# Performance work log

Hardware: AMD Instinct MI355X
Metric: run time of the kernel (lower is better)

## Reference

```python
import jax, jax.numpy as jnp
import numpy as np

B, L, C, S, W, R = 2, 16, 64, 64, 128, 32
MOD_HIDDEN = 32


def _conv3d(x, k, b, pad_hw):
    # x: (B,C,L,S,W), k: (O,I,1,kh,kw)
    y = jax.lax.conv_general_dilated(
        x, k, window_strides=(1, 1, 1),
        padding=((0, 0), (pad_hw, pad_hw), (pad_hw, pad_hw)),
        dimension_numbers=('NCDHW', 'OIDHW', 'NCDHW'))
    return y + b[None, :, None, None, None]


def setup_inputs() -> dict:
    key = jax.random.key(0)
    ks = jax.random.split(key, 16)
    d = {}
    d['x'] = jax.random.normal(ks[0], (B, L, C, S, W), jnp.float32)
    u1 = jax.random.uniform(ks[1], (C, R), jnp.float32)
    u2 = jax.random.uniform(ks[2], (C, R), jnp.float32)
    r_min, r_max = 0.8, 0.99
    d['nu_log'] = jnp.log(-0.5 * jnp.log(u1 * (r_max ** 2 - r_min ** 2) + r_min ** 2))
    d['theta_log'] = jnp.log(u2 * jnp.float32(2 * np.pi))
    d['disp_nu'] = jnp.zeros((C, R), jnp.float32)
    d['disp_theta'] = jnp.zeros((C, R), jnp.float32)
    d['mlp_w1'] = jax.random.normal(ks[3], (C, MOD_HIDDEN), jnp.float32) / np.sqrt(C).astype(np.float32)
    d['mlp_b1'] = jnp.zeros((MOD_HIDDEN,), jnp.float32)
    d['mlp_w2'] = jax.random.normal(ks[4], (MOD_HIDDEN, C * R * 2), jnp.float32) / np.sqrt(MOD_HIDDEN).astype(np.float32)
    d['mlp_b2'] = jnp.zeros((C * R * 2,), jnp.float32)
    d['forcing_scale'] = jnp.float32(0.1)
    d['U_row_r'] = jax.random.normal(ks[5], (C, S, R), jnp.float32) / np.sqrt(S).astype(np.float32)
    d['U_row_i'] = jax.random.normal(ks[6], (C, S, R), jnp.float32) / np.sqrt(S).astype(np.float32)
    d['V_col_r'] = jax.random.normal(ks[7], (C, W, R), jnp.float32) / np.sqrt(W).astype(np.float32)
    d['V_col_i'] = jax.random.normal(ks[8], (C, W, R), jnp.float32) / np.sqrt(W).astype(np.float32)
    d['proj_W_r'] = jax.random.normal(ks[9], (C, C), jnp.float32) / np.sqrt(C).astype(np.float32)
    d['proj_W_i'] = jax.random.normal(ks[10], (C, C), jnp.float32) / np.sqrt(C).astype(np.float32)
    d['proj_b_r'] = jnp.zeros((C,), jnp.float32)
    d['proj_b_i'] = jnp.zeros((C,), jnp.float32)
    fan = np.sqrt(C * 9).astype(np.float32)
    d['convr_k'] = jax.random.normal(ks[11], (C, C, 1, 3, 3), jnp.float32) / fan
    d['convr_b'] = jnp.zeros((C,), jnp.float32)
    d['convi_k'] = jax.random.normal(ks[12], (C, C, 1, 3, 3), jnp.float32) / fan
    d['convi_b'] = jnp.zeros((C,), jnp.float32)
    d['fuse_k'] = jax.random.normal(ks[13], (C, 2 * C, 1, 1, 1), jnp.float32) / np.sqrt(2 * C).astype(np.float32)
    d['fuse_b'] = jnp.zeros((C,), jnp.float32)
    d['ln_g'] = jnp.ones((S, W), jnp.float32)
    d['ln_b'] = jnp.zeros((S, W), jnp.float32)
    return d


def reference(x, nu_log, theta_log, disp_nu, disp_theta, mlp_w1, mlp_b1,
              mlp_w2, mlp_b2, forcing_scale, U_row_r, U_row_i, V_col_r,
              V_col_i, proj_W_r, proj_W_i, proj_b_r, proj_b_i, convr_k,
              convr_b, convi_k, convi_b, fuse_k, fuse_b, ln_g, ln_b):
    # Diagonal LRU poles lam = exp(-exp(nu) + i*exp(theta)), per (C,R)
    nu = jnp.exp(nu_log + disp_nu)
    theta = jnp.exp(theta_log + disp_theta)
    lam = jnp.exp(jax.lax.complex(-nu, theta))
    gamma = jnp.sqrt(jnp.clip(1.0 - jnp.abs(lam) ** 2, 1e-6, None))

    # Selective input-dependent forcing from spatially-pooled context
    ctx = x.mean(axis=(-2, -1))  # (B,L,C)
    f = jnp.tanh(ctx @ mlp_w1 + mlp_b1) @ mlp_w2 + mlp_b2
    f = f.reshape(ctx.shape[0], ctx.shape[1], C, R, 2)
    forcing = forcing_scale * jax.lax.complex(f[..., 0], f[..., 1])  # (B,L,C,R)

    # Low-rank complex spatial projection to rank-R state per channel
    U = jax.lax.complex(U_row_r, U_row_i)  # (C,S,R)
    V = jax.lax.complex(V_col_r, V_col_i)  # (C,W,R)
    xc = x.astype(jnp.complex64)
    u = jnp.einsum('blcsw,csr->blcwr', xc, jnp.conj(U))
    u = jnp.einsum('blcwr,cwr->blcr', u, jnp.conj(V))  # (B,L,C,R)
    u = gamma * u * (1.0 + forcing)

    # Diagonal linear recurrence h_t = lam*h_{t-1} + u_t via associative scan over L
    A = jnp.broadcast_to(lam[None, None], u.shape)

    def comb(e1, e2):
        a1, b1 = e1
        a2, b2 = e2
        return a1 * a2, a2 * b1 + b2

    _, h = jax.lax.associative_scan(comb, (A, u), axis=1)

    # Reconstruct spatial field from low-rank states
    t = jnp.einsum('blcr,csr->blcsr', h, U)
    y = jnp.einsum('blcsr,cwr->blcsw', t, V)  # (B,L,C,S,W) complex

    projW = jax.lax.complex(proj_W_r, proj_W_i)
    projb = jax.lax.complex(proj_b_r, proj_b_i)
    y = jnp.einsum('blcsw,oc->blosw', y, projW) + projb[None, None, :, None, None]

    # Post-recurrence spatial convs on real/imag parts, fuse, layernorm, residual
    yr = jnp.transpose(jnp.real(y), (0, 2, 1, 3, 4))  # (B,C,L,S,W)
    yi = jnp.transpose(jnp.imag(y), (0, 2, 1, 3, 4))
    yr = _conv3d(yr, convr_k, convr_b, 1)
    yi = _conv3d(yi, convi_k, convi_b, 1)
    fused = _conv3d(jnp.concatenate([yr, yi], axis=1), fuse_k, fuse_b, 0)
    fused = jnp.transpose(fused, (0, 2, 1, 3, 4))  # (B,L,C,S,W)

    mu = fused.mean(axis=(-2, -1), keepdims=True)
    var = fused.var(axis=(-2, -1), keepdims=True)
    normed = (fused - mu) / jnp.sqrt(var + 1e-5) * ln_g + ln_b
    return normed + x
```

## Files before the change

kernel.cpp:

```cpp
#include <hip/hip_runtime.h>

typedef unsigned short u16;
typedef unsigned int u32;
typedef __attribute__((ext_vector_type(8))) short short8;
typedef __attribute__((ext_vector_type(4))) float f32x4;
typedef __attribute__((ext_vector_type(16))) float f32x16;

constexpr int B = 2, L = 16, C = 64, S = 64, W = 128, R = 32, MH = 32;
constexpr int BL = B * L;
constexpr int SW = S * W;
constexpr int CR = C * R;
constexpr int F2 = C * R * 2;

__device__ __forceinline__ float us2f(u16 h) { return __uint_as_float(((u32)h) << 16); }
__device__ __forceinline__ float bf_lo(u32 u) { return __uint_as_float(u << 16); }
__device__ __forceinline__ float bf_hi(u32 u) { return __uint_as_float(u & 0xffff0000u); }
__device__ __forceinline__ u16 f2bu(float f) {
  u32 u = __float_as_uint(f);
  u32 r = (u + 0x7fffu + ((u >> 16) & 1u)) >> 16;
  return (u16)r;
}
__device__ __forceinline__ u32 pack2(float lo, float hi) {
  return (u32)f2bu(lo) | ((u32)f2bu(hi) << 16);
}

__global__ void k_prep(const float* __restrict__ nu_log, const float* __restrict__ th_log,
                       const float* __restrict__ dnu, const float* __restrict__ dth,
                       float* __restrict__ lamr, float* __restrict__ lami,
                       float* __restrict__ gam) {
  int i = blockIdx.x * 256 + threadIdx.x;
  if (i >= CR) return;
  float nu = expf(nu_log[i] + dnu[i]);
  float th = expf(th_log[i] + dth[i]);
  float mag = expf(-nu);
  lamr[i] = mag * cosf(th);
  lami[i] = mag * sinf(th);
  gam[i] = sqrtf(fmaxf(1.0f - mag * mag, 1e-6f));
}

__global__ void k_keff(const float* __restrict__ fuse_k, const float* __restrict__ fuse_b,
                       const float* __restrict__ convr_k, const float* __restrict__ convr_b,
                       const float* __restrict__ convi_k, const float* __restrict__ convi_b,
                       u16* __restrict__ keff_bf, float* __restrict__ biaseff) {
  int i = blockIdx.x * 256 + threadIdx.x;
  if (i < C * 2 * C * 9) {
    int o = i / (2 * C * 9);
    int rem = i - o * (2 * C * 9);
    int cin2 = rem / 9;
    int seg = rem - cin2 * 9;
    const float* ck = (cin2 < C) ? convr_k : convi_k;
    int cin = cin2 & (C - 1);
    int fbase = o * 2 * C + ((cin2 < C) ? 0 : C);
    float acc = 0.f;
    for (int m = 0; m < C; ++m)
      acc += fuse_k[fbase + m] * ck[(m * C + cin) * 9 + seg];
    int kslice = cin2 >> 4;
    int kk = cin2 & 15;
    int lane = (o & 31) | ((kk >> 3) << 5);
    int j = kk & 7;
    int m_tile = o >> 5;
    keff_bf[((((seg * 8 + kslice) * 2 + m_tile) * 64 + lane) << 3) + j] = f2bu(acc);
  } else if (i < C * 2 * C * 9 + C) {
    int o = i - C * 2 * C * 9;
    float acc = fuse_b[o];
    for (int m = 0; m < C; ++m) {
      acc += fuse_k[o * 2 * C + m] * convr_b[m];
      acc += fuse_k[o * 2 * C + C + m] * convi_b[m];
    }
    biaseff[o] = acc;
  }
}

__global__ void k_apack(const float* __restrict__ pWr, const float* __restrict__ pWi,
                        u16* __restrict__ aproj) {
  int i = blockIdx.x * 256 + threadIdx.x;
  if (i >= 128 * 128) return;
  int m = i >> 7, k = i & 127;
  int c = k >> 1, im = k & 1;
  int o = m & 63;
  float v;
  if (m < 64) v = im ? -pWi[o * 64 + c] : pWr[o * 64 + c];
  else        v = im ?  pWr[o * 64 + c] : pWi[o * 64 + c];
  aproj[i] = f2bu(v);
}

__global__ __launch_bounds__(256) void k_mlp(
    const float* __restrict__ ctx, const float* __restrict__ w1, const float* __restrict__ b1,
    const float* __restrict__ w2, const float* __restrict__ b2, const float* __restrict__ fscale,
    float* __restrict__ forcing) {
  int bl = blockIdx.x >> 4;
  int kt = blockIdx.x & 15;
  int k0 = kt * 256;
  __shared__ float cv[C];
  __shared__ float hid[MH];
  __shared__ float lw2[MH * 256];
  int t = threadIdx.x;
  if (t < C) cv[t] = ctx[bl * C + t];
  for (int i = t; i < MH * 64; i += 256) {
    int j = i >> 6, q = i & 63;
    ((float4*)lw2)[i] = ((const float4*)(w2 + (size_t)j * F2 + k0))[q];
  }
  __syncthreads();
  if (t < MH) {
    float a = b1[t];
    for (int c2 = 0; c2 < C; ++c2) a += cv[c2] * w1[c2 * MH + t];
    hid[t] = tanhf(a);
  }
  __syncthreads();
  float scale = fscale[0];
  float a = b2[k0 + t];
#pragma unroll
  for (int j = 0; j < MH; ++j) a += hid[j] * lw2[j * 256 + t];
  forcing[(size_t)bl * F2 + k0 + t] = scale * a;
}

__global__ __launch_bounds__(256) void k_enc(
    const float* __restrict__ x,
    const float* __restrict__ Vr, const float* __restrict__ Vi,
    const float* __restrict__ Ur, const float* __restrict__ Ui,
    float* __restrict__ ctx, float* __restrict__ u) {
  int blc = blockIdx.x;
  int c = blc & (C - 1);
  __shared__ __align__(16) char smem[17408 * 2 + 16384 + 64];
  u16* xt = (u16*)smem;
  u16* bt = (u16*)(smem + 17408);
  float* uldr = (float*)(smem + 34816);
  float* uldi = uldr + 2048;
  float* y1  = (float*)smem;
  float* part = (float*)(smem + 17408);
  float* red = (float*)(smem + 17408 * 2 + 16384);
  int t = threadIdx.x;
  int lane = t & 63, wv = t >> 6;
  float sm = 0.f;
  {
    const float4* xp = (const float4*)(x + (size_t)blc * SW);
    for (int i = t; i < SW / 4; i += 256) {
      float4 v = xp[i];
      sm += v.x + v.y + v.z + v.w;
      int idx = i * 4, s = idx >> 7, w = idx & 127;
      u32* d = (u32*)&xt[s * 136 + w];
      d[0] = pack2(v.x, v.y);
      d[1] = pack2(v.z, v.w);
    }
  }
#pragma unroll
  for (int o = 32; o > 0; o >>= 1) sm += __shfl_down(sm, o, 64);
  if (lane == 0) red[wv] = sm;
  {
    const float* vrp = Vr + (size_t)c * 4096;
    const float* vip = Vi + (size_t)c * 4096;
    for (int i = t; i < 4096; i += 256) {
      int w = i >> 5, r = i & 31;
      bt[r * 136 + w]        = f2bu(vrp[i]);
      bt[(32 + r) * 136 + w] = f2bu(-vip[i]);
    }
  }
  {
    const float* urp = Ur + (size_t)c * 2048;
    const float* uip = Ui + (size_t)c * 2048;
    for (int i = t; i < 2048; i += 256) { uldr[i] = urp[i]; uldi[i] = uip[i]; }
  }
  __syncthreads();
  if (t == 0) ctx[blc] = (red[0] + red[1] + red[2] + red[3]) * (1.f / SW);
  int quad = lane >> 4, l15 = lane & 15;
  f32x4 zf = {0.f, 0.f, 0.f, 0.f};
  f32x4 acc[4] = {zf, zf, zf, zf};
#pragma unroll
  for (int ks = 0; ks < 4; ++ks) {
    int kofs = ks * 32 + quad * 8;
    short8 bf = *(const short8*)&bt[(wv * 16 + l15) * 136 + kofs];
#pragma unroll
    for (int mt = 0; mt < 4; ++mt) {
      short8 af = *(const short8*)&xt[(mt * 16 + l15) * 136 + kofs];
      acc[mt] = __builtin_amdgcn_mfma_f32_16x16x32_bf16(af, bf, acc[mt], 0, 0, 0);
    }
  }
  __syncthreads();
#pragma unroll
  for (int mt = 0; mt < 4; ++mt)
#pragma unroll
    for (int reg = 0; reg < 4; ++reg)
      y1[(mt * 16 + quad * 4 + reg) * 65 + wv * 16 + l15] = acc[mt][reg];
  __syncthreads();
  {
    int r = t & 31, sg = t >> 5;
    float pr = 0.f, pi = 0.f;
#pragma unroll
    for (int k = 0; k < 8; ++k) {
      int s = sg * 8 + k;
      float yr = y1[s * 65 + r], yi = y1[s * 65 + 32 + r];
      float ur = uldr[s * 32 + r], ui = uldi[s * 32 + r];
      pr += ur * yr + ui * yi;
      pi += ur * yi - ui * yr;
    }
    part[sg * 64 + r * 2]     = pr;
    part[sg * 64 + r * 2 + 1] = pi;
  }
  __syncthreads();
  if (t < 32) {
    float pr = 0.f, pi = 0.f;
#pragma unroll
    for (int sg = 0; sg < 8; ++sg) {
      pr += part[sg * 64 + t * 2];
      pi += part[sg * 64 + t * 2 + 1];
    }
    u[((size_t)blc * R + t) * 2]     = pr;
    u[((size_t)blc * R + t) * 2 + 1] = pi;
  }
}

__global__ void k_scan(const float* __restrict__ lamr, const float* __restrict__ lami,
                       const float* __restrict__ gam, const float* __restrict__ forcing,
                       const float* __restrict__ u, float* __restrict__ h) {
  int i = blockIdx.x * 256 + threadIdx.x;
  if (i >= B * CR) return;
  int b = i / CR;
  int cr = i - b * CR;
  float lr = lamr[cr], li = lami[cr], g = gam[cr];
  float hr = 0.f, hi = 0.f;
  for (int l = 0; l < L; ++l) {
    size_t off = ((size_t)(b * L + l) * CR + cr) * 2;
    float ur0 = u[off], ui0 = u[off + 1];
    float fr = forcing[off], fi = forcing[off + 1];
    float ofr = 1.f + fr;
    float ur = g * (ur0 * ofr - ui0 * fi);
    float ui = g * (ur0 * fi + ui0 * ofr);
    float nr = lr * hr - li * hi + ur;
    float ni = lr * hi + li * hr + ui;
    hr = nr; hi = ni;
    h[off] = hr; h[off + 1] = hi;
  }
}

__global__ __launch_bounds__(256) void k_decode(
    const float* __restrict__ h,
    const float* __restrict__ Ur, const float* __restrict__ Ui,
    const float* __restrict__ Vr, const float* __restrict__ Vi,
    u32* __restrict__ y_cm32, int bl_base) {
  int bid = blockIdx.x;
  int c = bid & 63;
  int blh = bid >> 6;
  int bl = bl_base + blh;
  __shared__ __align__(16) u16 ldA[64 * 72];
  __shared__ __align__(16) u16 ldBr[128 * 72];
  __shared__ __align__(16) u16 ldBi[128 * 72];
  int t = threadIdx.x;
  {
    const float* hp = h + ((size_t)(bl * C + c) * R) * 2;
    const float* urp = Ur + (size_t)c * (S * R);
    const float* uip = Ui + (size_t)c * (S * R);
    for (int p = t; p < S * R; p += 256) {
      int s = p >> 5, r = p & 31;
      float hr = hp[r * 2], hi = hp[r * 2 + 1];
      float ur = urp[p], ui = uip[p];
      ldA[s * 72 + r]      = f2bu(hr * ur - hi * ui);
      ldA[s * 72 + 32 + r] = f2bu(hr * ui + hi * ur);
    }
  }
  {
    const float* vrp = Vr + (size_t)c * (W * R);
    const float* vip = Vi + (size_t)c * (W * R);
    for (int p = t; p < W * R; p += 256) {
      int w = p >> 5, r = p & 31;
      float vr = vrp[p], vi = vip[p];
      ldBr[w * 72 + r]      = f2bu(vr);
      ldBr[w * 72 + 32 + r] = f2bu(-vi);
      ldBi[w * 72 + r]      = f2bu(vi);
      ldBi[w * 72 + 32 + r] = f2bu(vr);
    }
  }
  __syncthreads();
  int lane = t & 63, q = t >> 6;
  int quad = lane >> 4, l15 = lane & 15;
  f32x4 zf = {0.f, 0.f, 0.f, 0.f};
  f32x4 accr[4][2], acci[4][2];
#pragma unroll
  for (int mt = 0; mt < 4; ++mt)
#pragma unroll
    for (int nt = 0; nt < 2; ++nt) { accr[mt][nt] = zf; acci[mt][nt] = zf; }
#pragma unroll
  for (int ks = 0; ks < 2; ++ks) {
    int kofs = ks * 32 + quad * 8;
    short8 af[4];
#pragma unroll
    for (int mt = 0; mt < 4; ++mt)
      af[mt] = *(const short8*)&ldA[(mt * 16 + l15) * 72 + kofs];
#pragma unroll
    for (int nt = 0; nt < 2; ++nt) {
      int wrow = q * 32 + nt * 16 + l15;
      short8 br = *(const short8*)&ldBr[wrow * 72 + kofs];
      short8 bi = *(const short8*)&ldBi[wrow * 72 + kofs];
#pragma unroll
      for (int mt = 0; mt < 4; ++mt) {
        accr[mt][nt] = __builtin_amdgcn_mfma_f32_16x16x32_bf16(af[mt], br, accr[mt][nt], 0, 0, 0);
        acci[mt][nt] = __builtin_amdgcn_mfma_f32_16x16x32_bf16(af[mt], bi, acci[mt][nt], 0, 0, 0);
      }
    }
  }
  u32* dst = y_cm32 + ((size_t)(blh * 64 + c) << 13);
#pragma unroll
  for (int mt = 0; mt < 4; ++mt) {
#pragma unroll
    for (int nt = 0; nt < 2; ++nt) {
      int w = q * 32 + nt * 16 + l15;
#pragma unroll
      for (int reg = 0; reg < 4; ++reg) {
        int s = mt * 16 + quad * 4 + reg;
        dst[s * 128 + w] = pack2(accr[mt][nt][reg], acci[mt][nt][reg]);
      }
    }
  }
}

__global__ __launch_bounds__(256) void k_proj(
    const u32* __restrict__ y_cm32, const u16* __restrict__ aproj,
    const float* __restrict__ pbr, const float* __restrict__ pbi,
    u16* __restrict__ ynhwc, int bl_base) {
  int bid = blockIdx.x;
  int ntile = bid & 15;
  int blh = bid >> 4;
  int bl = bl_base + blh;
  __shared__ __align__(16) u16 lda[128 * 136];
  __shared__ __align__(16) u32 ldb[128 * 68];
  __shared__ float ldbias[128];
  int t = threadIdx.x;
  for (int i = t; i < 128 * 16; i += 256) {
    int m = i >> 4, qq = i & 15;
    ((uint4*)&lda[m * 136])[qq] = ((const uint4*)&aproj[m * 128])[qq];
  }
  if (t < 128) ldbias[t] = t < 64 ? pbr[t] : pbi[t - 64];

  int lane = t & 63, wv = t >> 6;
  int quad = lane >> 4, l15 = lane & 15;
  int cidx = t & 63, seg = t >> 6;
  f32x4 zf = {0.f, 0.f, 0.f, 0.f};

  for (int chunk = 0; chunk < 4; ++chunk) {
    int n0 = ntile * 512 + chunk * 128;
    __syncthreads();
    {
      const uint4* src = (const uint4*)(y_cm32 + (((size_t)(blh * 64 + cidx)) << 13) + n0 + seg * 32);
      u32 tmp[32];
#pragma unroll
      for (int qq = 0; qq < 8; ++qq) {
        uint4 v = src[qq];
        tmp[qq * 4] = v.x; tmp[qq * 4 + 1] = v.y; tmp[qq * 4 + 2] = v.z; tmp[qq * 4 + 3] = v.w;
      }
#pragma unroll
      for (int j = 0; j < 32; ++j)
        ldb[(seg * 32 + j) * 68 + cidx] = tmp[j];
    }
    __syncthreads();
    f32x4 acc[8][2];
#pragma unroll
    for (int mt = 0; mt < 8; ++mt) { acc[mt][0] = zf; acc[mt][1] = zf; }
    const u16* ldb16 = (const u16*)ldb;
#pragma unroll
    for (int ks = 0; ks < 4; ++ks) {
      int kofs = ks * 32 + quad * 8;
      short8 af[8];
#pragma unroll
      for (int mt = 0; mt < 8; ++mt)
        af[mt] = *(const short8*)&lda[(mt * 16 + l15) * 136 + kofs];
#pragma unroll
      for (int nt = 0; nt < 2; ++nt) {
        int nrow = wv * 32 + nt * 16 + l15;
        short8 bf = *(const short8*)&ldb16[nrow * 136 + kofs];
#pragma unroll
        for (int mt = 0; mt < 8; ++mt)
          acc[mt][nt] = __builtin_amdgcn_mfma_f32_16x16x32_bf16(af[mt], bf, acc[mt][nt], 0, 0, 0);
      }
    }
#pragma unroll
    for (int nt = 0; nt < 2; ++nt) {
      int n = n0 + wv * 32 + nt * 16 + l15;
      u16* drow = ynhwc + (((size_t)bl * SW + n) << 7);
#pragma unroll
      for (int mt = 0; mt < 8; ++mt) {
        int ch = mt * 16 + quad * 4;
        u32 lo = pack2(acc[mt][nt][0] + ldbias[ch],     acc[mt][nt][1] + ldbias[ch + 1]);
        u32 hi = pack2(acc[mt][nt][2] + ldbias[ch + 2], acc[mt][nt][3] + ldbias[ch + 3]);
        u32* dp = (u32*)(drow + ch);
        dp[0] = lo; dp[1] = hi;
      }
    }
  }
}

__global__ __launch_bounds__(256, 4) void k_conv(
    const u16* __restrict__ ynhwc, const u16* __restrict__ keff_bf,
    const float* __restrict__ biaseff, u16* __restrict__ fused) {
  int bid = blockIdx.x;
  int wt = bid & 1;
  int st = (bid >> 1) & 31;
  int bl = bid >> 6;
  int s0 = st * 2;
  int w0 = wt * 64;
  __shared__ __align__(16) u16 win[4][66][72];
  int t = threadIdx.x;
  int c_lo = (wt == 0) ? 1 : 0;
  int c_hi = (wt == 0) ? 66 : 65;
  uint4 z4 = make_uint4(0u, 0u, 0u, 0u);

  int lane = t & 63;
  int wv = t >> 6;
  int sr = wv & 1;
  int mt = wv >> 1;
  int l31 = lane & 31, khalf = lane >> 5;

  f32x16 acc0, acc1;
#pragma unroll
  for (int i = 0; i < 16; ++i) { acc0[i] = 0.f; acc1[i] = 0.f; }
  const short8* ap = (const short8*)keff_bf;
  short8 abuf[2];

#pragma unroll
  for (int p = 0; p < 2; ++p) {
    if (p) __syncthreads();
    for (int rr = 0; rr < 4; ++rr) {
      int rs = s0 - 1 + rr;
      if (rs < 0 || rs >= S) {
        for (int i = t; i < 66 * 8; i += 256) {
          int col = i >> 3, q = i & 7;
          ((uint4*)&win[rr][col][0])[q] = z4;
        }
      } else {
        if (wt == 0 && t < 8) ((uint4*)&win[rr][0][0])[t] = z4;
        if (wt == 1 && t < 8) ((uint4*)&win[rr][65][0])[t] = z4;
        const uint4* src = (const uint4*)(ynhwc +
            (((size_t)bl * S + rs) * W + (w0 - 1 + c_lo)) * 128 + p * 64);
        int n4 = (c_hi - c_lo) * 8;
        for (int i = t; i < n4; i += 256) {
          int col = i >> 3, q = i & 7;
          ((uint4*)&win[rr][c_lo + col][0])[q] = src[col * 16 + q];
        }
      }
    }
    __syncthreads();

    abuf[0] = ap[((p * 4) * 2 + mt) * 64 + lane];

#pragma unroll
    for (int m = 0; m < 36; ++m) {
      const int cur = m & 1;
      const int nxt = cur ^ 1;
      if (m < 35) {
        const int m1 = m + 1;
        abuf[nxt] = ap[((((m1 >> 2) * 8 + p * 4 + (m1 & 3)) * 2 + mt)) * 64 + lane];
      }
      const int seg = m >> 2;
      const int k4 = m & 3;
      const int dr = seg / 3;
      const int dc = seg - dr * 3;
      const u16* bb = &win[sr + dr][l31 + dc][k4 * 16 + khalf * 8];
      short8 b0 = *(const short8*)bb;
      short8 b1 = *(const short8*)(bb + 32 * 72);
      acc0 = __builtin_amdgcn_mfma_f32_32x32x16_bf16(abuf[cur], b0, acc0, 0, 0, 0);
      acc1 = __builtin_amdgcn_mfma_f32_32x32x16_bf16(abuf[cur], b1, acc1, 0, 0, 0);
    }
  }

  int s_out = s0 + sr;
#pragma unroll
  for (int reg = 0; reg < 16; ++reg) {
    int o = mt * 32 + (reg & 3) + 8 * (reg >> 2) + 4 * khalf;
    float bias = biaseff[o];
    size_t rowoff = ((size_t)(bl * C + o) * S + s_out) * W;
    fused[rowoff + w0 + l31]      = f2bu(acc0[reg] + bias);
    fused[rowoff + w0 + 32 + l31] = f2bu(acc1[reg] + bias);
  }
}

__global__ __launch_bounds__(256) void k_ln(
    const u16* __restrict__ fused,
    const float* __restrict__ ln_g, const float* __restrict__ ln_b,
    const float* __restrict__ x, float* __restrict__ out) {
  int blc = blockIdx.x;
  __shared__ u16 fs[SW];
  __shared__ float red[12];
  int t = threadIdx.x;
  const uint4* fp = (const uint4*)(fused + (size_t)blc * SW);
  float sm = 0.f, sq = 0.f;
  for (int i = t; i < SW / 8; i += 256) {
    uint4 v = fp[i];
    ((uint4*)fs)[i] = v;
    float f0 = bf_lo(v.x), f1 = bf_hi(v.x), f2 = bf_lo(v.y), f3 = bf_hi(v.y);
    float f4 = bf_lo(v.z), f5 = bf_hi(v.z), f6 = bf_lo(v.w), f7 = bf_hi(v.w);
    sm += f0 + f1 + f2 + f3 + f4 + f5 + f6 + f7;
    sq += f0 * f0 + f1 * f1 + f2 * f2 + f3 * f3 + f4 * f4 + f5 * f5 + f6 * f6 + f7 * f7;
  }
#pragma unroll
  for (int off = 32; off > 0; off >>= 1) {
    sm += __shfl_down(sm, off, 64);
    sq += __shfl_down(sq, off, 64);
  }
  int lane = t & 63, wid = t >> 6;
  if (lane == 0) { red[wid * 2] = sm; red[wid * 2 + 1] = sq; }
  __syncthreads();
  if (t == 0) {
    float S1 = red[0] + red[2] + red[4] + red[6];
    float S2 = red[1] + red[3] + red[5] + red[7];
    float mu = S1 * (1.f / SW);
    float var = S2 * (1.f / SW) - mu * mu;
    red[8] = mu;
    red[9] = rsqrtf(var + 1e-5f);
  }
  __syncthreads();
  float mu = red[8], rstd = red[9];
  const float4* xp4 = (const float4*)(x + (size_t)blc * SW);
  float4* op4 = (float4*)(out + (size_t)blc * SW);
  const float4* g4 = (const float4*)ln_g;
  const float4* b4 = (const float4*)ln_b;
  const uint2* fs2 = (const uint2*)fs;
  for (int i = t; i < SW / 4; i += 256) {
    uint2 fv = fs2[i];
    float4 xv = xp4[i];
    float4 gv = g4[i];
    float4 bv = b4[i];
    float4 o;
    o.x = (bf_lo(fv.x) - mu) * rstd * gv.x + bv.x + xv.x;
    o.y = (bf_hi(fv.x) - mu) * rstd * gv.y + bv.y + xv.y;
    o.z = (bf_lo(fv.y) - mu) * rstd * gv.z + bv.z + xv.z;
    o.w = (bf_hi(fv.y) - mu) * rstd * gv.w + bv.w + xv.w;
    op4[i] = o;
  }
}

extern "C" void kernel_launch(void* const* d_in, const int* in_sizes, int n_in,
                              void* d_out, int out_size, void* d_ws, size_t ws_size,
                              hipStream_t stream) {
  (void)in_sizes; (void)n_in; (void)out_size; (void)ws_size;
  const float* x       = (const float*)d_in[0];
  const float* nu_log  = (const float*)d_in[1];
  const float* th_log  = (const float*)d_in[2];
  const float* dnu     = (const float*)d_in[3];
  const float* dth     = (const float*)d_in[4];
  const float* w1      = (const float*)d_in[5];
  const float* b1      = (const float*)d_in[6];
  const float* w2      = (const float*)d_in[7];
  const float* b2      = (const float*)d_in[8];
  const float* fscale  = (const float*)d_in[9];
  const float* Ur      = (const float*)d_in[10];
  const float* Ui      = (const float*)d_in[11];
  const float* Vr      = (const float*)d_in[12];
  const float* Vi      = (const float*)d_in[13];
  const float* pWr     = (const float*)d_in[14];
  const float* pWi     = (const float*)d_in[15];
  const float* pbr     = (const float*)d_in[16];
  const float* pbi     = (const float*)d_in[17];
  const float* convr_k = (const float*)d_in[18];
  const float* convr_b = (const float*)d_in[19];
  const float* convi_k = (const float*)d_in[20];
  const float* convi_b = (const float*)d_in[21];
  const float* fuse_k  = (const float*)d_in[22];
  const float* fuse_b  = (const float*)d_in[23];
  const float* ln_g    = (const float*)d_in[24];
  const float* ln_b    = (const float*)d_in[25];
  float* out = (float*)d_out;

  char* ws = (char*)d_ws;
  float* lamr    = (float*)ws;
  float* lami    = lamr + 2048;
  float* gam     = lami + 2048;
  float* biaseff = gam + 2048;
  float* ctx     = biaseff + 64;
  float* forcing = ctx + 2048;
  float* ubuf    = forcing + 131072;
  float* hbuf    = ubuf + 131072;
  u16* keff_bf   = (u16*)(hbuf + 131072);
  u16* aproj     = keff_bf + 73728;
  size_t off = ((size_t)((char*)(aproj + 16384) - ws) + 255) & ~(size_t)255;
  u32* y_cm32    = (u32*)(ws + off);
  u16* fused     = (u16*)y_cm32;
  u16* ynhwc     = (u16*)(ws + off + (size_t)32 * 1024 * 1024);

  k_prep<<<8, 256, 0, stream>>>(nu_log, th_log, dnu, dth, lamr, lami, gam);
  k_keff<<<289, 256, 0, stream>>>(fuse_k, fuse_b, convr_k, convr_b, convi_k, convi_b,
                                  keff_bf, biaseff);
  k_apack<<<64, 256, 0, stream>>>(pWr, pWi, aproj);
  k_enc<<<BL * C, 256, 0, stream>>>(x, Vr, Vi, Ur, Ui, ctx, ubuf);
  k_mlp<<<BL * 16, 256, 0, stream>>>(ctx, w1, b1, w2, b2, fscale, forcing);
  k_scan<<<16, 256, 0, stream>>>(lamr, lami, gam, forcing, ubuf, hbuf);
  k_decode<<<1024, 256, 0, stream>>>(hbuf, Ur, Ui, Vr, Vi, y_cm32, 0);
  k_proj<<<256, 256, 0, stream>>>(y_cm32, aproj, pbr, pbi, ynhwc, 0);
  k_decode<<<1024, 256, 0, stream>>>(hbuf, Ur, Ui, Vr, Vi, y_cm32, 16);
  k_proj<<<256, 256, 0, stream>>>(y_cm32, aproj, pbr, pbi, ynhwc, 16);
  k_conv<<<2048, 256, 0, stream>>>(ynhwc, keff_bf, biaseff, fused);
  k_ln<<<BL * C, 256, 0, stream>>>(fused, ln_g, ln_b, x, out);
}
```

Baseline: 344.0 us.

## Prepack V weights into MFMA fragment layout once, load directly in enc/decode

Adds a k_vpack kernel that converts Vr/Vi to bf16 and arranges them in the exact per-lane MFMA B-fragment order for both the encoder and the decoder. k_enc and k_decode now load those fragments straight from global memory into registers. This removes the per-block fp32 load, convert and LDS transpose of V that was repeated across 2048 blocks each, and it shrinks LDS use. The cost is one extra launch of 6144 blocks and some extra workspace.

```diff
diff --git a/kernel.cpp b/kernel.cpp
--- a/kernel.cpp
+++ b/kernel.cpp
@@ -11,6 +11,8 @@
 constexpr int SW = S * W;
 constexpr int CR = C * R;
 constexpr int F2 = C * R * 2;
+constexpr int NVE = 64 * 4 * 4 * 64 * 8;
+constexpr int NVD = 64 * 8 * 2 * 64 * 8;
 
 __device__ __forceinline__ float us2f(u16 h) { return __uint_as_float(((u32)h) << 16); }
 __device__ __forceinline__ float bf_lo(u32 u) { return __uint_as_float(u << 16); }
@@ -71,6 +73,35 @@
   }
 }
 
+__global__ void k_vpack(const float* __restrict__ Vr, const float* __restrict__ Vi,
+                        u16* __restrict__ venc, u16* __restrict__ vdecr,
+                        u16* __restrict__ vdeci) {
+  int i = blockIdx.x * 256 + threadIdx.x;
+  if (i < NVE) {
+    int j = i & 7, lane = (i >> 3) & 63, ks = (i >> 9) & 3;
+    int wv = (i >> 11) & 3, c = i >> 13;
+    int n = wv * 16 + (lane & 15);
+    int w = ks * 32 + ((lane >> 4) & 3) * 8 + j;
+    float v = (n < 32) ? Vr[(size_t)c * 4096 + w * 32 + n]
+                       : -Vi[(size_t)c * 4096 + w * 32 + (n - 32)];
+    venc[i] = f2bu(v);
+  } else if (i < NVE + 2 * NVD) {
+    int ii = i - NVE;
+    int isI = 0;
+    if (ii >= NVD) { ii -= NVD; isI = 1; }
+    int j = ii & 7, lane = (ii >> 3) & 63, ks = (ii >> 9) & 1;
+    int g = (ii >> 10) & 7, c = ii >> 13;
+    int w = g * 16 + (lane & 15);
+    int k = ks * 32 + ((lane >> 4) & 3) * 8 + j;
+    float v;
+    if (!isI) v = (k < 32) ? Vr[(size_t)c * 4096 + w * 32 + k]
+                           : -Vi[(size_t)c * 4096 + w * 32 + (k - 32)];
+    else      v = (k < 32) ? Vi[(size_t)c * 4096 + w * 32 + k]
+                           :  Vr[(size_t)c * 4096 + w * 32 + (k - 32)];
+    (isI ? vdeci : vdecr)[ii] = f2bu(v);
+  }
+}
+
 __global__ void k_apack(const float* __restrict__ pWr, const float* __restrict__ pWi,
                         u16* __restrict__ aproj) {
   int i = blockIdx.x * 256 + threadIdx.x;
@@ -115,22 +146,26 @@
 }
 
 __global__ __launch_bounds__(256) void k_enc(
-    const float* __restrict__ x,
-    const float* __restrict__ Vr, const float* __restrict__ Vi,
+    const float* __restrict__ x, const u16* __restrict__ venc,
     const float* __restrict__ Ur, const float* __restrict__ Ui,
     float* __restrict__ ctx, float* __restrict__ u) {
   int blc = blockIdx.x;
   int c = blc & (C - 1);
-  __shared__ __align__(16) char smem[17408 * 2 + 16384 + 64];
+  __shared__ __align__(16) char smem[35968];
   u16* xt = (u16*)smem;
-  u16* bt = (u16*)(smem + 17408);
-  float* uldr = (float*)(smem + 34816);
+  float* uldr = (float*)(smem + 17408);
   float* uldi = uldr + 2048;
   float* y1  = (float*)smem;
-  float* part = (float*)(smem + 17408);
-  float* red = (float*)(smem + 17408 * 2 + 16384);
+  float* part = (float*)(smem + 33792);
+  float* red = (float*)(smem + 35840);
   int t = threadIdx.x;
   int lane = t & 63, wv = t >> 6;
+  short8 bf[4];
+  {
+    const short8* vep = (const short8*)venc + ((size_t)(c * 4 + wv) * 4) * 64 + lane;
+#pragma unroll
+    for (int ks = 0; ks < 4; ++ks) bf[ks] = vep[ks * 64];
+  }
   float sm = 0.f;
   {
     const float4* xp = (const float4*)(x + (size_t)blc * SW);
@@ -147,15 +182,6 @@
   for (int o = 32; o > 0; o >>= 1) sm += __shfl_down(sm, o, 64);
   if (lane == 0) red[wv] = sm;
   {
-    const float* vrp = Vr + (size_t)c * 4096;
-    const float* vip = Vi + (size_t)c * 4096;
-    for (int i = t; i < 4096; i += 256) {
-      int w = i >> 5, r = i & 31;
-      bt[r * 136 + w]        = f2bu(vrp[i]);
-      bt[(32 + r) * 136 + w] = f2bu(-vip[i]);
-    }
-  }
-  {
     const float* urp = Ur + (size_t)c * 2048;
     const float* uip = Ui + (size_t)c * 2048;
     for (int i = t; i < 2048; i += 256) { uldr[i] = urp[i]; uldi[i] = uip[i]; }
@@ -168,11 +194,10 @@
 #pragma unroll
   for (int ks = 0; ks < 4; ++ks) {
     int kofs = ks * 32 + quad * 8;
-    short8 bf = *(const short8*)&bt[(wv * 16 + l15) * 136 + kofs];
 #pragma unroll
     for (int mt = 0; mt < 4; ++mt) {
       short8 af = *(const short8*)&xt[(mt * 16 + l15) * 136 + kofs];
-      acc[mt] = __builtin_amdgcn_mfma_f32_16x16x32_bf16(af, bf, acc[mt], 0, 0, 0);
+      acc[mt] = __builtin_amdgcn_mfma_f32_16x16x32_bf16(af, bf[ks], acc[mt], 0, 0, 0);
     }
   }
   __syncthreads();
@@ -235,15 +260,13 @@
 __global__ __launch_bounds__(256) void k_decode(
     const float* __restrict__ h,
     const float* __restrict__ Ur, const float* __restrict__ Ui,
-    const float* __restrict__ Vr, const float* __restrict__ Vi,
+    const u16* __restrict__ vdecr, const u16* __restrict__ vdeci,
     u32* __restrict__ y_cm32, int bl_base) {
   int bid = blockIdx.x;
   int c = bid & 63;
   int blh = bid >> 6;
   int bl = bl_base + blh;
   __shared__ __align__(16) u16 ldA[64 * 72];
-  __shared__ __align__(16) u16 ldBr[128 * 72];
-  __shared__ __align__(16) u16 ldBi[128 * 72];
   int t = threadIdx.x;
   {
     const float* hp = h + ((size_t)(bl * C + c) * R) * 2;
@@ -257,21 +280,11 @@
       ldA[s * 72 + 32 + r] = f2bu(hr * ui + hi * ur);
     }
   }
-  {
-    const float* vrp = Vr + (size_t)c * (W * R);
-    const float* vip = Vi + (size_t)c * (W * R);
-    for (int p = t; p < W * R; p += 256) {
-      int w = p >> 5, r = p & 31;
-      float vr = vrp[p], vi = vip[p];
-      ldBr[w * 72 + r]      = f2bu(vr);
-      ldBr[w * 72 + 32 + r] = f2bu(-vi);
-      ldBi[w * 72 + r]      = f2bu(vi);
-      ldBi[w * 72 + 32 + r] = f2bu(vr);
-    }
-  }
   __syncthreads();
   int lane = t & 63, q = t >> 6;
   int quad = lane >> 4, l15 = lane & 15;
+  const short8* vdr = (const short8*)vdecr + (size_t)c * 16 * 64;
+  const short8* vdi = (const short8*)vdeci + (size_t)c * 16 * 64;
   f32x4 zf = {0.f, 0.f, 0.f, 0.f};
   f32x4 accr[4][2], acci[4][2];
 #pragma unroll
@@ -287,9 +300,9 @@
       af[mt] = *(const short8*)&ldA[(mt * 16 + l15) * 72 + kofs];
 #pragma unroll
     for (int nt = 0; nt < 2; ++nt) {
-      int wrow = q * 32 + nt * 16 + l15;
-      short8 br = *(const short8*)&ldBr[wrow * 72 + kofs];
-      short8 bi = *(const short8*)&ldBi[wrow * 72 + kofs];
+      int g = q * 2 + nt;
+      short8 br = vdr[(g * 2 + ks) * 64 + lane];
+      short8 bi = vdi[(g * 2 + ks) * 64 + lane];
 #pragma unroll
       for (int mt = 0; mt < 4; ++mt) {
         accr[mt][nt] = __builtin_amdgcn_mfma_f32_16x16x32_bf16(af[mt], br, accr[mt][nt], 0, 0, 0);
@@ -569,7 +582,10 @@
   float* hbuf    = ubuf + 131072;
   u16* keff_bf   = (u16*)(hbuf + 131072);
   u16* aproj     = keff_bf + 73728;
-  size_t off = ((size_t)((char*)(aproj + 16384) - ws) + 255) & ~(size_t)255;
+  u16* venc      = aproj + 16384;
+  u16* vdecr     = venc + NVE;
+  u16* vdeci     = vdecr + NVD;
+  size_t off = ((size_t)((char*)(vdeci + NVD) - ws) + 255) & ~(size_t)255;
   u32* y_cm32    = (u32*)(ws + off);
   u16* fused     = (u16*)y_cm32;
   u16* ynhwc     = (u16*)(ws + off + (size_t)32 * 1024 * 1024);
@@ -577,13 +593,14 @@
   k_prep<<<8, 256, 0, stream>>>(nu_log, th_log, dnu, dth, lamr, lami, gam);
   k_keff<<<289, 256, 0, stream>>>(fuse_k, fuse_b, convr_k, convr_b, convi_k, convi_b,
                                   keff_bf, biaseff);
+  k_vpack<<<6144, 256, 0, stream>>>(Vr, Vi, venc, vdecr, vdeci);
   k_apack<<<64, 256, 0, stream>>>(pWr, pWi, aproj);
-  k_enc<<<BL * C, 256, 0, stream>>>(x, Vr, Vi, Ur, Ui, ctx, ubuf);
+  k_enc<<<BL * C, 256, 0, stream>>>(x, venc, Ur, Ui, ctx, ubuf);
   k_mlp<<<BL * 16, 256, 0, stream>>>(ctx, w1, b1, w2, b2, fscale, forcing);
   k_scan<<<16, 256, 0, stream>>>(lamr, lami, gam, forcing, ubuf, hbuf);
-  k_decode<<<1024, 256, 0, stream>>>(hbuf, Ur, Ui, Vr, Vi, y_cm32, 0);
+  k_decode<<<1024, 256, 0, stream>>>(hbuf, Ur, Ui, vdecr, vdeci, y_cm32, 0);
   k_proj<<<256, 256, 0, stream>>>(y_cm32, aproj, pbr, pbi, ynhwc, 0);
-  k_decode<<<1024, 256, 0, stream>>>(hbuf, Ur, Ui, Vr, Vi, y_cm32, 16);
+  k_decode<<<1024, 256, 0, stream>>>(hbuf, Ur, Ui, vdecr, vdeci, y_cm32, 16);
   k_proj<<<256, 256, 0, stream>>>(y_cm32, aproj, pbr, pbi, ynhwc, 16);
   k_conv<<<2048, 256, 0, stream>>>(ynhwc, keff_bf, biaseff, fused);
   k_ln<<<BL * C, 256, 0, stream>>>(fused, ln_g, ln_b, x, out);
```

After: 338.8 us. Within noise of the previous version (-1.5%).
